# Optimization experiments

Measured on AMD Instinct MI355X. Metric: run time of the kernel, lower is better.

Reference implementation:

```python
import jax, jax.numpy as jnp
import numpy as np

B, S, E, Q, A = 32, 2048, 1024, 1024, 512

def setup_inputs() -> dict:
    key = jax.random.key(0)
    k1, k2, k3, k4, k5 = jax.random.split(key, 5)
    scale = lambda d: 1.0 / np.sqrt(d)
    return {
        "inputs": jax.random.normal(k1, (B, S, E), dtype=jnp.float32),
        "query": jax.random.normal(k2, (B, Q), dtype=jnp.float32),
        "W_in": jax.random.normal(k3, (E, A), dtype=jnp.float32) * scale(E),
        "W_q": jax.random.normal(k4, (Q, A), dtype=jnp.float32) * scale(Q),
        "w_att": jax.random.normal(k5, (A,), dtype=jnp.float32) * scale(A),
    }

def reference(inputs, query, W_in, W_q, w_att):
    # projected inputs: [B, S, A]
    proj_in = jnp.einsum("bse,ea->bsa", inputs, W_in)
    # projected query, broadcast over S: [B, 1, A]
    proj_q = (query @ W_q)[:, None, :]
    # additive scores: [B, S]
    scores = jnp.einsum("bsa,a->bs", jnp.tanh(proj_in + proj_q), w_att)
    weights = jax.nn.softmax(scores, axis=1)  # over sequence dim
    # context over PROJECTED inputs (as in original): [B, A]
    context = jnp.einsum("bs,bsa->ba", weights, proj_in)
    return context
```

## Files before the change

### kernel.cpp

```cpp
#include <hip/hip_runtime.h>
#include <hip/hip_fp16.h>
#include <cstdint>
#include <cstddef>

#define Bb 32
#define Ss 2048
#define Ee 1024
#define Qq 1024
#define Aa 512

typedef _Float16 half8 __attribute__((ext_vector_type(8)));
typedef _Float16 half4 __attribute__((ext_vector_type(4)));
typedef __fp16 fp16x2 __attribute__((ext_vector_type(2)));
typedef float f32x4 __attribute__((ext_vector_type(4)));

#define WS_PROJQ 0u
#define WS_MPART 65536u
#define WS_LPART 67584u
#define WS_CTXP  69632u
#define WS_WWS   1118208u

__device__ __forceinline__ float fast_tanh(float x) {
  float e = __expf(2.0f * x);
  return 1.0f - __fdividef(2.0f, e + 1.0f);
}

__device__ __forceinline__ half4 cvt4(float4 x) {
  fp16x2 lo = __builtin_amdgcn_cvt_pkrtz(x.x, x.y);
  fp16x2 hi = __builtin_amdgcn_cvt_pkrtz(x.z, x.w);
  half4 r;
  r[0] = (_Float16)lo[0]; r[1] = (_Float16)lo[1];
  r[2] = (_Float16)hi[0]; r[3] = (_Float16)hi[1];
  return r;
}

__global__ void k_convw(const float* __restrict__ win, _Float16* __restrict__ wws) {
  int gid = blockIdx.x * 256 + threadIdx.x;
  int a  = gid & 511;
  int ks = (gid >> 9) & 3;
  int kt = gid >> 11;
  int k0 = kt * 32 + ks * 8;
  half8 v;
  #pragma unroll
  for (int j = 0; j < 8; ++j) v[j] = (_Float16)win[(size_t)(k0 + j) * Aa + a];
  *(half8*)(wws + ((size_t)kt * 16384 + (size_t)ks * 4096 + (size_t)a * 8)) = v;
}

__global__ void k_projq(const float* __restrict__ query, const float* __restrict__ wq,
                        float* __restrict__ projq) {
  __shared__ float red[256];
  int b  = blockIdx.y;
  int al = threadIdx.x & 63;
  int eq = threadIdx.x >> 6;
  int a  = blockIdx.x * 64 + al;
  const float* q = query + (size_t)b * Qq;
  float s = 0.f;
  int e0 = eq * 256;
  #pragma unroll 4
  for (int e = e0; e < e0 + 256; ++e)
    s += q[e] * wq[(size_t)e * Aa + a];
  red[threadIdx.x] = s;
  __syncthreads();
  if (eq == 0)
    projq[(size_t)b * Aa + a] = red[al] + red[al + 64] + red[al + 128] + red[al + 192];
}

__global__ __launch_bounds__(1024, 4)
void k_main(const float* __restrict__ inp, const _Float16* __restrict__ wws,
            const float* __restrict__ projq, const float* __restrict__ watt,
            float* __restrict__ mpart, float* __restrict__ lpart,
            float* __restrict__ ctxp)
{
  __shared__ __align__(16) _Float16 Alds[2][4 * 128 * 8];
  __shared__ __align__(16) _Float16 Blds[2][4 * 512 * 8];
  __shared__ float pq_s[512];
  __shared__ float wa_s[512];
  __shared__ float sc4[128][4];
  __shared__ float pbuf[128];
  __shared__ float red2[8];
  __shared__ float ctx2[4][512];

  const int tid = threadIdx.x;
  const int l   = tid & 63;
  const int w   = tid >> 6;
  const int lr  = l & 15;
  const int kb  = l >> 4;
  const int wr  = w >> 2;
  const int wc  = w & 3;
  const int b   = blockIdx.y;
  const int ch  = blockIdx.x;

  if (tid < 512) {
    pq_s[tid] = projq[(size_t)b * Aa + tid];
    wa_s[tid] = watt[tid];
  }

  const int arow = tid >> 3;
  const int kq   = tid & 7;
  const float* asrc = inp + ((size_t)(b * Ss + ch * 128 + arow)) * Ee + kq * 4;
  const int awoff = ((kq >> 1) * 128 + arow) * 8 + (kq & 1) * 4;

  const char* bsrc0 = (const char*)wws + (size_t)tid * 16;

  f32x4 acc[2][8];
  #pragma unroll
  for (int m = 0; m < 2; ++m)
    #pragma unroll
    for (int n = 0; n < 8; ++n) acc[m][n] = (f32x4){0.f, 0.f, 0.f, 0.f};

  {
    float4 x = *(const float4*)(asrc);
    *(half4*)(Alds[0] + awoff) = cvt4(x);
    #pragma unroll
    for (int i = 0; i < 2; ++i)
      __builtin_amdgcn_global_load_lds(
        (const __attribute__((address_space(1))) void*)(bsrc0 + i * 16384),
        (__attribute__((address_space(3))) void*)((char*)Blds[0] + tid * 16 + i * 16384),
        16, 0, 0);
  }
  float4 areg = *(const float4*)(asrc + 32);
  __syncthreads();

  int p = 0;
  for (int kt = 0; kt < 32; ++kt) {
    if (kt < 31) {
      const char* bs = bsrc0 + (size_t)(kt + 1) * 32768;
      #pragma unroll
      for (int i = 0; i < 2; ++i)
        __builtin_amdgcn_global_load_lds(
          (const __attribute__((address_space(1))) void*)(bs + i * 16384),
          (__attribute__((address_space(3))) void*)((char*)Blds[p ^ 1] + tid * 16 + i * 16384),
          16, 0, 0);
    }
    const int ktn2 = (kt < 30) ? kt + 2 : 31;
    float4 anext = *(const float4*)(asrc + (size_t)ktn2 * 32);

    half8 af0 = *(const half8*)(Alds[p] + (kb * 128 + wr * 32 +      lr) * 8);
    half8 af1 = *(const half8*)(Alds[p] + (kb * 128 + wr * 32 + 16 + lr) * 8);
    const _Float16* Bp = Blds[p] + (kb * 512 + wc * 128 + lr) * 8;
    half8 bf0 = *(const half8*)(Bp);
    half8 bf1 = *(const half8*)(Bp + 16 * 8);
    half8 bf2 = *(const half8*)(Bp + 32 * 8);
    half8 bf3 = *(const half8*)(Bp + 48 * 8);

    acc[0][0] = __builtin_amdgcn_mfma_f32_16x16x32_f16(af0, bf0, acc[0][0], 0, 0, 0);
    acc[1][0] = __builtin_amdgcn_mfma_f32_16x16x32_f16(af1, bf0, acc[1][0], 0, 0, 0);
    acc[0][1] = __builtin_amdgcn_mfma_f32_16x16x32_f16(af0, bf1, acc[0][1], 0, 0, 0);
    acc[1][1] = __builtin_amdgcn_mfma_f32_16x16x32_f16(af1, bf1, acc[1][1], 0, 0, 0);
    acc[0][2] = __builtin_amdgcn_mfma_f32_16x16x32_f16(af0, bf2, acc[0][2], 0, 0, 0);
    acc[1][2] = __builtin_amdgcn_mfma_f32_16x16x32_f16(af1, bf2, acc[1][2], 0, 0, 0);
    acc[0][3] = __builtin_amdgcn_mfma_f32_16x16x32_f16(af0, bf3, acc[0][3], 0, 0, 0);
    acc[1][3] = __builtin_amdgcn_mfma_f32_16x16x32_f16(af1, bf3, acc[1][3], 0, 0, 0);

    half8 bf4 = *(const half8*)(Bp + 64 * 8);
    half8 bf5 = *(const half8*)(Bp + 80 * 8);
    half8 bf6 = *(const half8*)(Bp + 96 * 8);
    half8 bf7 = *(const half8*)(Bp + 112 * 8);
    acc[0][4] = __builtin_amdgcn_mfma_f32_16x16x32_f16(af0, bf4, acc[0][4], 0, 0, 0);
    acc[1][4] = __builtin_amdgcn_mfma_f32_16x16x32_f16(af1, bf4, acc[1][4], 0, 0, 0);
    acc[0][5] = __builtin_amdgcn_mfma_f32_16x16x32_f16(af0, bf5, acc[0][5], 0, 0, 0);
    acc[1][5] = __builtin_amdgcn_mfma_f32_16x16x32_f16(af1, bf5, acc[1][5], 0, 0, 0);
    acc[0][6] = __builtin_amdgcn_mfma_f32_16x16x32_f16(af0, bf6, acc[0][6], 0, 0, 0);
    acc[1][6] = __builtin_amdgcn_mfma_f32_16x16x32_f16(af1, bf6, acc[1][6], 0, 0, 0);
    acc[0][7] = __builtin_amdgcn_mfma_f32_16x16x32_f16(af0, bf7, acc[0][7], 0, 0, 0);
    acc[1][7] = __builtin_amdgcn_mfma_f32_16x16x32_f16(af1, bf7, acc[1][7], 0, 0, 0);

    if (kt < 31) {
      *(half4*)(Alds[p ^ 1] + awoff) = cvt4(areg);
    }
    __syncthreads();
    p ^= 1;
    areg = anext;
  }

  float sp[2][4];
  #pragma unroll
  for (int m = 0; m < 2; ++m)
    #pragma unroll
    for (int j = 0; j < 4; ++j) sp[m][j] = 0.f;

  #pragma unroll
  for (int n = 0; n < 8; ++n) {
    int col = wc * 128 + n * 16 + lr;
    float wan = wa_s[col], pqn = pq_s[col];
    #pragma unroll
    for (int m = 0; m < 2; ++m)
      #pragma unroll
      for (int j = 0; j < 4; ++j)
        sp[m][j] += fast_tanh(acc[m][n][j] + pqn) * wan;
  }
  #pragma unroll
  for (int m = 0; m < 2; ++m)
    #pragma unroll
    for (int j = 0; j < 4; ++j) {
      float v = sp[m][j];
      v += __shfl_xor(v, 1);
      v += __shfl_xor(v, 2);
      v += __shfl_xor(v, 4);
      v += __shfl_xor(v, 8);
      sp[m][j] = v;
    }
  if (lr == 0) {
    #pragma unroll
    for (int m = 0; m < 2; ++m)
      #pragma unroll
      for (int j = 0; j < 4; ++j)
        sc4[wr * 32 + m * 16 + kb * 4 + j][wc] = sp[m][j];
  }
  __syncthreads();

  const int pi = b * 16 + ch;
  float s = 0.f, pe = 0.f;
  if (tid < 128) {
    s = sc4[tid][0] + sc4[tid][1] + sc4[tid][2] + sc4[tid][3];
    float mx = s;
    #pragma unroll
    for (int off = 1; off < 64; off <<= 1) mx = fmaxf(mx, __shfl_xor(mx, off));
    if (l == 0) red2[w] = mx;
  }
  __syncthreads();
  float Mx = fmaxf(red2[0], red2[1]);
  if (tid < 128) {
    pe = __expf(s - Mx);
    pbuf[tid] = pe;
    float ls = pe;
    #pragma unroll
    for (int off = 1; off < 64; off <<= 1) ls += __shfl_xor(ls, off);
    if (l == 0) red2[4 + w] = ls;
  }
  __syncthreads();
  if (tid == 0) { mpart[pi] = Mx; lpart[pi] = red2[4] + red2[5]; }

  float cv[8];
  #pragma unroll
  for (int n = 0; n < 8; ++n) cv[n] = 0.f;
  #pragma unroll
  for (int m = 0; m < 2; ++m)
    #pragma unroll
    for (int j = 0; j < 4; ++j) {
      float pw = pbuf[wr * 32 + m * 16 + kb * 4 + j];
      #pragma unroll
      for (int n = 0; n < 8; ++n) cv[n] += pw * acc[m][n][j];
    }
  #pragma unroll
  for (int n = 0; n < 8; ++n) {
    float v = cv[n];
    v += __shfl_xor(v, 16);
    v += __shfl_xor(v, 32);
    cv[n] = v;
  }
  if (l < 16) {
    #pragma unroll
    for (int n = 0; n < 8; ++n) ctx2[wr][wc * 128 + n * 16 + l] = cv[n];
  }
  __syncthreads();

  if (tid < 512)
    ctxp[(size_t)pi * 512 + tid] =
        ctx2[0][tid] + ctx2[1][tid] + ctx2[2][tid] + ctx2[3][tid];
}

__global__ void k_comb(const float* __restrict__ mpart, const float* __restrict__ lpart,
                       const float* __restrict__ ctxp, float* __restrict__ out) {
  int b = blockIdx.x, a = threadIdx.x;
  float Mg = -1e30f;
  #pragma unroll
  for (int i = 0; i < 16; ++i) Mg = fmaxf(Mg, mpart[b * 16 + i]);
  float den = 0.f, s = 0.f;
  #pragma unroll
  for (int i = 0; i < 16; ++i) {
    float e = __expf(mpart[b * 16 + i] - Mg);
    den += lpart[b * 16 + i] * e;
    s   += ctxp[((size_t)(b * 16 + i)) * 512 + a] * e;
  }
  out[(size_t)b * 512 + a] = s / den;
}

extern "C" void kernel_launch(void* const* d_in, const int* in_sizes, int n_in,
                              void* d_out, int out_size, void* d_ws, size_t ws_size,
                              hipStream_t stream) {
  const float* inputs = (const float*)d_in[0];
  const float* query  = (const float*)d_in[1];
  const float* W_in   = (const float*)d_in[2];
  const float* W_q    = (const float*)d_in[3];
  const float* w_att  = (const float*)d_in[4];
  float* out = (float*)d_out;

  char* ws = (char*)d_ws;
  float*    projq = (float*)(ws + WS_PROJQ);
  float*    mpart = (float*)(ws + WS_MPART);
  float*    lpart = (float*)(ws + WS_LPART);
  float*    ctxp  = (float*)(ws + WS_CTXP);
  _Float16* wws   = (_Float16*)(ws + WS_WWS);

  k_convw<<<256, 256, 0, stream>>>(W_in, wws);
  k_projq<<<dim3(8, 32), 256, 0, stream>>>(query, W_q, projq);
  k_main<<<dim3(16, 32), 1024, 0, stream>>>(inputs, wws, projq, w_att, mpart, lpart, ctxp);
  k_comb<<<32, 512, 0, stream>>>(mpart, lpart, ctxp, out);
}
```

Measured before the change: 137.2 us.

## Merge prep kernels and reshape warp tiling to 64x64 per wave

The two small prep kernels (W_in fp16 conversion and query projection) become one launch with branches keyed on block index. In the main kernel the 16 waves change from a 4x4 grid of 32x128 tiles to a 2x8 grid of 64x64 tiles. Each wave now loads 4 A and 4 B fragments per k-step instead of 2 A and 8 B, which lowers LDS read traffic per MFMA. The epilogue is adjusted to match, with 8-way score partials and 2-way context partials.

New measurement: 134.6 us, median of 2. Within noise of the previous version (-1.9%).

```diff
diff --git a/kernel.cpp b/kernel.cpp
--- a/kernel.cpp
+++ b/kernel.cpp
@@ -34,35 +34,38 @@
   return r;
 }
 
-__global__ void k_convw(const float* __restrict__ win, _Float16* __restrict__ wws) {
-  int gid = blockIdx.x * 256 + threadIdx.x;
-  int a  = gid & 511;
-  int ks = (gid >> 9) & 3;
-  int kt = gid >> 11;
-  int k0 = kt * 32 + ks * 8;
-  half8 v;
-  #pragma unroll
-  for (int j = 0; j < 8; ++j) v[j] = (_Float16)win[(size_t)(k0 + j) * Aa + a];
-  *(half8*)(wws + ((size_t)kt * 16384 + (size_t)ks * 4096 + (size_t)a * 8)) = v;
-}
-
-__global__ void k_projq(const float* __restrict__ query, const float* __restrict__ wq,
-                        float* __restrict__ projq) {
-  __shared__ float red[256];
-  int b  = blockIdx.y;
-  int al = threadIdx.x & 63;
-  int eq = threadIdx.x >> 6;
-  int a  = blockIdx.x * 64 + al;
-  const float* q = query + (size_t)b * Qq;
-  float s = 0.f;
-  int e0 = eq * 256;
-  #pragma unroll 4
-  for (int e = e0; e < e0 + 256; ++e)
-    s += q[e] * wq[(size_t)e * Aa + a];
-  red[threadIdx.x] = s;
-  __syncthreads();
-  if (eq == 0)
-    projq[(size_t)b * Aa + a] = red[al] + red[al + 64] + red[al + 128] + red[al + 192];
+__global__ void k_prep(const float* __restrict__ win, _Float16* __restrict__ wws,
+                       const float* __restrict__ query, const float* __restrict__ wq,
+                       float* __restrict__ projq) {
+  if (blockIdx.x < 256) {
+    int gid = blockIdx.x * 256 + threadIdx.x;
+    int a  = gid & 511;
+    int ks = (gid >> 9) & 3;
+    int kt = gid >> 11;
+    int k0 = kt * 32 + ks * 8;
+    half8 v;
+    #pragma unroll
+    for (int j = 0; j < 8; ++j) v[j] = (_Float16)win[(size_t)(k0 + j) * Aa + a];
+    *(half8*)(wws + ((size_t)kt * 16384 + (size_t)ks * 4096 + (size_t)a * 8)) = v;
+  } else {
+    __shared__ float red[256];
+    int pb = blockIdx.x - 256;
+    int b  = pb >> 3;
+    int ax = pb & 7;
+    int al = threadIdx.x & 63;
+    int eq = threadIdx.x >> 6;
+    int a  = ax * 64 + al;
+    const float* q = query + (size_t)b * Qq;
+    float s = 0.f;
+    int e0 = eq * 256;
+    #pragma unroll 4
+    for (int e = e0; e < e0 + 256; ++e)
+      s += q[e] * wq[(size_t)e * Aa + a];
+    red[threadIdx.x] = s;
+    __syncthreads();
+    if (eq == 0)
+      projq[(size_t)b * Aa + a] = red[al] + red[al + 64] + red[al + 128] + red[al + 192];
+  }
 }
 
 __global__ __launch_bounds__(1024, 4)
@@ -75,18 +78,18 @@
   __shared__ __align__(16) _Float16 Blds[2][4 * 512 * 8];
   __shared__ float pq_s[512];
   __shared__ float wa_s[512];
-  __shared__ float sc4[128][4];
+  __shared__ float sc8[128][8];
   __shared__ float pbuf[128];
   __shared__ float red2[8];
-  __shared__ float ctx2[4][512];
+  __shared__ float ctx2[2][512];
 
   const int tid = threadIdx.x;
   const int l   = tid & 63;
   const int w   = tid >> 6;
   const int lr  = l & 15;
   const int kb  = l >> 4;
-  const int wr  = w >> 2;
-  const int wc  = w & 3;
+  const int wr  = w >> 3;
+  const int wc  = w & 7;
   const int b   = blockIdx.y;
   const int ch  = blockIdx.x;
 
@@ -102,11 +105,11 @@
 
   const char* bsrc0 = (const char*)wws + (size_t)tid * 16;
 
-  f32x4 acc[2][8];
-  #pragma unroll
-  for (int m = 0; m < 2; ++m)
-    #pragma unroll
-    for (int n = 0; n < 8; ++n) acc[m][n] = (f32x4){0.f, 0.f, 0.f, 0.f};
+  f32x4 acc[4][4];
+  #pragma unroll
+  for (int m = 0; m < 4; ++m)
+    #pragma unroll
+    for (int n = 0; n < 4; ++n) acc[m][n] = (f32x4){0.f, 0.f, 0.f, 0.f};
 
   {
     float4 x = *(const float4*)(asrc);
@@ -135,35 +138,32 @@
     const int ktn2 = (kt < 30) ? kt + 2 : 31;
     float4 anext = *(const float4*)(asrc + (size_t)ktn2 * 32);
 
-    half8 af0 = *(const half8*)(Alds[p] + (kb * 128 + wr * 32 +      lr) * 8);
-    half8 af1 = *(const half8*)(Alds[p] + (kb * 128 + wr * 32 + 16 + lr) * 8);
-    const _Float16* Bp = Blds[p] + (kb * 512 + wc * 128 + lr) * 8;
+    half8 af0 = *(const half8*)(Alds[p] + (kb * 128 + wr * 64 +      lr) * 8);
+    half8 af1 = *(const half8*)(Alds[p] + (kb * 128 + wr * 64 + 16 + lr) * 8);
+    half8 af2 = *(const half8*)(Alds[p] + (kb * 128 + wr * 64 + 32 + lr) * 8);
+    half8 af3 = *(const half8*)(Alds[p] + (kb * 128 + wr * 64 + 48 + lr) * 8);
+    const _Float16* Bp = Blds[p] + (kb * 512 + wc * 64 + lr) * 8;
     half8 bf0 = *(const half8*)(Bp);
     half8 bf1 = *(const half8*)(Bp + 16 * 8);
     half8 bf2 = *(const half8*)(Bp + 32 * 8);
     half8 bf3 = *(const half8*)(Bp + 48 * 8);
 
     acc[0][0] = __builtin_amdgcn_mfma_f32_16x16x32_f16(af0, bf0, acc[0][0], 0, 0, 0);
+    acc[0][1] = __builtin_amdgcn_mfma_f32_16x16x32_f16(af0, bf1, acc[0][1], 0, 0, 0);
+    acc[0][2] = __builtin_amdgcn_mfma_f32_16x16x32_f16(af0, bf2, acc[0][2], 0, 0, 0);
+    acc[0][3] = __builtin_amdgcn_mfma_f32_16x16x32_f16(af0, bf3, acc[0][3], 0, 0, 0);
     acc[1][0] = __builtin_amdgcn_mfma_f32_16x16x32_f16(af1, bf0, acc[1][0], 0, 0, 0);
-    acc[0][1] = __builtin_amdgcn_mfma_f32_16x16x32_f16(af0, bf1, acc[0][1], 0, 0, 0);
     acc[1][1] = __builtin_amdgcn_mfma_f32_16x16x32_f16(af1, bf1, acc[1][1], 0, 0, 0);
-    acc[0][2] = __builtin_amdgcn_mfma_f32_16x16x32_f16(af0, bf2, acc[0][2], 0, 0, 0);
     acc[1][2] = __builtin_amdgcn_mfma_f32_16x16x32_f16(af1, bf2, acc[1][2], 0, 0, 0);
-    acc[0][3] = __builtin_amdgcn_mfma_f32_16x16x32_f16(af0, bf3, acc[0][3], 0, 0, 0);
     acc[1][3] = __builtin_amdgcn_mfma_f32_16x16x32_f16(af1, bf3, acc[1][3], 0, 0, 0);
-
-    half8 bf4 = *(const half8*)(Bp + 64 * 8);
-    half8 bf5 = *(const half8*)(Bp + 80 * 8);
-    half8 bf6 = *(const half8*)(Bp + 96 * 8);
-    half8 bf7 = *(const half8*)(Bp + 112 * 8);
-    acc[0][4] = __builtin_amdgcn_mfma_f32_16x16x32_f16(af0, bf4, acc[0][4], 0, 0, 0);
-    acc[1][4] = __builtin_amdgcn_mfma_f32_16x16x32_f16(af1, bf4, acc[1][4], 0, 0, 0);
-    acc[0][5] = __builtin_amdgcn_mfma_f32_16x16x32_f16(af0, bf5, acc[0][5], 0, 0, 0);
-    acc[1][5] = __builtin_amdgcn_mfma_f32_16x16x32_f16(af1, bf5, acc[1][5], 0, 0, 0);
-    acc[0][6] = __builtin_amdgcn_mfma_f32_16x16x32_f16(af0, bf6, acc[0][6], 0, 0, 0);
-    acc[1][6] = __builtin_amdgcn_mfma_f32_16x16x32_f16(af1, bf6, acc[1][6], 0, 0, 0);
-    acc[0][7] = __builtin_amdgcn_mfma_f32_16x16x32_f16(af0, bf7, acc[0][7], 0, 0, 0);
-    acc[1][7] = __builtin_amdgcn_mfma_f32_16x16x32_f16(af1, bf7, acc[1][7], 0, 0, 0);
+    acc[2][0] = __builtin_amdgcn_mfma_f32_16x16x32_f16(af2, bf0, acc[2][0], 0, 0, 0);
+    acc[2][1] = __builtin_amdgcn_mfma_f32_16x16x32_f16(af2, bf1, acc[2][1], 0, 0, 0);
+    acc[2][2] = __builtin_amdgcn_mfma_f32_16x16x32_f16(af2, bf2, acc[2][2], 0, 0, 0);
+    acc[2][3] = __builtin_amdgcn_mfma_f32_16x16x32_f16(af2, bf3, acc[2][3], 0, 0, 0);
+    acc[3][0] = __builtin_amdgcn_mfma_f32_16x16x32_f16(af3, bf0, acc[3][0], 0, 0, 0);
+    acc[3][1] = __builtin_amdgcn_mfma_f32_16x16x32_f16(af3, bf1, acc[3][1], 0, 0, 0);
+    acc[3][2] = __builtin_amdgcn_mfma_f32_16x16x32_f16(af3, bf2, acc[3][2], 0, 0, 0);
+    acc[3][3] = __builtin_amdgcn_mfma_f32_16x16x32_f16(af3, bf3, acc[3][3], 0, 0, 0);
 
     if (kt < 31) {
       *(half4*)(Alds[p ^ 1] + awoff) = cvt4(areg);
@@ -173,24 +173,24 @@
     areg = anext;
   }
 
-  float sp[2][4];
-  #pragma unroll
-  for (int m = 0; m < 2; ++m)
+  float sp[4][4];
+  #pragma unroll
+  for (int m = 0; m < 4; ++m)
     #pragma unroll
     for (int j = 0; j < 4; ++j) sp[m][j] = 0.f;
 
   #pragma unroll
-  for (int n = 0; n < 8; ++n) {
-    int col = wc * 128 + n * 16 + lr;
+  for (int n = 0; n < 4; ++n) {
+    int col = wc * 64 + n * 16 + lr;
     float wan = wa_s[col], pqn = pq_s[col];
     #pragma unroll
-    for (int m = 0; m < 2; ++m)
+    for (int m = 0; m < 4; ++m)
       #pragma unroll
       for (int j = 0; j < 4; ++j)
         sp[m][j] += fast_tanh(acc[m][n][j] + pqn) * wan;
   }
   #pragma unroll
-  for (int m = 0; m < 2; ++m)
+  for (int m = 0; m < 4; ++m)
     #pragma unroll
     for (int j = 0; j < 4; ++j) {
       float v = sp[m][j];
@@ -202,17 +202,18 @@
     }
   if (lr == 0) {
     #pragma unroll
-    for (int m = 0; m < 2; ++m)
+    for (int m = 0; m < 4; ++m)
       #pragma unroll
       for (int j = 0; j < 4; ++j)
-        sc4[wr * 32 + m * 16 + kb * 4 + j][wc] = sp[m][j];
+        sc8[wr * 64 + m * 16 + kb * 4 + j][wc] = sp[m][j];
   }
   __syncthreads();
 
   const int pi = b * 16 + ch;
   float s = 0.f, pe = 0.f;
   if (tid < 128) {
-    s = sc4[tid][0] + sc4[tid][1] + sc4[tid][2] + sc4[tid][3];
+    s = sc8[tid][0] + sc8[tid][1] + sc8[tid][2] + sc8[tid][3]
+      + sc8[tid][4] + sc8[tid][5] + sc8[tid][6] + sc8[tid][7];
     float mx = s;
     #pragma unroll
     for (int off = 1; off < 64; off <<= 1) mx = fmaxf(mx, __shfl_xor(mx, off));
@@ -231,19 +232,19 @@
   __syncthreads();
   if (tid == 0) { mpart[pi] = Mx; lpart[pi] = red2[4] + red2[5]; }
 
-  float cv[8];
-  #pragma unroll
-  for (int n = 0; n < 8; ++n) cv[n] = 0.f;
-  #pragma unroll
-  for (int m = 0; m < 2; ++m)
+  float cv[4];
+  #pragma unroll
+  for (int n = 0; n < 4; ++n) cv[n] = 0.f;
+  #pragma unroll
+  for (int m = 0; m < 4; ++m)
     #pragma unroll
     for (int j = 0; j < 4; ++j) {
-      float pw = pbuf[wr * 32 + m * 16 + kb * 4 + j];
-      #pragma unroll
-      for (int n = 0; n < 8; ++n) cv[n] += pw * acc[m][n][j];
-    }
-  #pragma unroll
-  for (int n = 0; n < 8; ++n) {
+      float pw = pbuf[wr * 64 + m * 16 + kb * 4 + j];
+      #pragma unroll
+      for (int n = 0; n < 4; ++n) cv[n] += pw * acc[m][n][j];
+    }
+  #pragma unroll
+  for (int n = 0; n < 4; ++n) {
     float v = cv[n];
     v += __shfl_xor(v, 16);
     v += __shfl_xor(v, 32);
@@ -251,13 +252,12 @@
   }
   if (l < 16) {
     #pragma unroll
-    for (int n = 0; n < 8; ++n) ctx2[wr][wc * 128 + n * 16 + l] = cv[n];
+    for (int n = 0; n < 4; ++n) ctx2[wr][wc * 64 + n * 16 + l] = cv[n];
   }
   __syncthreads();
 
   if (tid < 512)
-    ctxp[(size_t)pi * 512 + tid] =
-        ctx2[0][tid] + ctx2[1][tid] + ctx2[2][tid] + ctx2[3][tid];
+    ctxp[(size_t)pi * 512 + tid] = ctx2[0][tid] + ctx2[1][tid];
 }
 
 __global__ void k_comb(const float* __restrict__ mpart, const float* __restrict__ lpart,
@@ -293,8 +293,7 @@
   float*    ctxp  = (float*)(ws + WS_CTXP);
   _Float16* wws   = (_Float16*)(ws + WS_WWS);
 
-  k_convw<<<256, 256, 0, stream>>>(W_in, wws);
-  k_projq<<<dim3(8, 32), 256, 0, stream>>>(query, W_q, projq);
+  k_prep<<<512, 256, 0, stream>>>(W_in, wws, query, W_q, projq);
   k_main<<<dim3(16, 32), 1024, 0, stream>>>(inputs, wws, projq, w_att, mpart, lpart, ctxp);
   k_comb<<<32, 512, 0, stream>>>(mpart, lpart, ctxp, out);
 }
```
